# Optimization experiments

Hardware: AMD Instinct MI355X
Metric: run time of the kernel (lower is better)

## Reference

```python
import jax, jax.numpy as jnp
import numpy as np

N = 100000   # nodes
E = 1600000  # edges (avg degree 16)
IN = 128
HID = 128


def _init_params(key):
    ks = jax.random.split(key, 3)
    def glorot(k, fan_in, fan_out):
        s = (6.0 / (fan_in + fan_out)) ** 0.5
        return jax.random.uniform(k, (fan_in, fan_out), jnp.float32, -s, s)
    W1 = glorot(ks[0], IN, HID)
    W_mu = glorot(ks[1], HID, HID)
    W_lv = glorot(ks[2], HID, HID)
    b1 = jnp.zeros((HID,), jnp.float32)
    b_mu = jnp.zeros((HID,), jnp.float32)
    b_lv = jnp.zeros((HID,), jnp.float32)
    return W1, b1, W_mu, b_mu, W_lv, b_lv


def setup_inputs() -> dict:
    key = jax.random.key(0)
    k_x, k_e, k_p = jax.random.split(key, 3)
    x = jax.random.normal(k_x, (N, IN), jnp.float32)
    edge_index = jax.random.randint(k_e, (2, E), 0, N, jnp.int32)
    W1, b1, W_mu, b_mu, W_lv, b_lv = _init_params(k_p)
    return {"x": x, "edge_index": edge_index,
            "W1": W1, "b1": b1, "W_mu": W_mu, "b_mu": b_mu,
            "W_lv": W_lv, "b_lv": b_lv}


def _gcn_conv(x, src, dst, coef, self_coef, W, b):
    # PyG GCNConv: h = X W;  out_i = sum_j norm_ji * h_j  (incl. self loop) + b
    h = x @ W                                   # [N, H] dense GEMM
    msg = h[src] * coef[:, None]                # gather + scale  [E, H]
    agg = jnp.zeros_like(h).at[dst].add(msg)    # scatter-add      [N, H]
    agg = agg + h * self_coef[:, None]          # self-loop contribution
    return agg + b


def reference(x, edge_index, W1, b1, W_mu, b_mu, W_lv, b_lv):
    src, dst = edge_index[0], edge_index[1]
    n = x.shape[0]
    # symmetric norm with self loops: deg_i = in_degree_i + 1
    deg = jnp.zeros((n,), x.dtype).at[dst].add(1.0) + 1.0
    dinv = jax.lax.rsqrt(deg)
    coef = dinv[src] * dinv[dst]                # per-edge norm
    self_coef = dinv * dinv                     # per-node self-loop norm

    h = jax.nn.elu(_gcn_conv(x, src, dst, coef, self_coef, W1, b1))
    mu = _gcn_conv(h, src, dst, coef, self_coef, W_mu, b_mu)
    logvar = _gcn_conv(h, src, dst, coef, self_coef, W_lv, b_lv)

    # reparameterize: z = mu + eps * exp(0.5*logvar)
    eps = jax.random.normal(jax.random.key(42), mu.shape, mu.dtype)
    z = mu + eps * jnp.exp(0.5 * logvar)
    return z, mu, logvar
```

## Files before the change

kernel.cpp:

```cpp
#include <hip/hip_runtime.h>
#include <hip/hip_bf16.h>
#include <cstring>
#include <cstdint>

#define N_NODES 100000
#define N_EDGES 1600000
#define HID 128
#define TOT (N_NODES * HID)
#define GEMM_GRID_C 782
#define SCAT_GRID_C 6250



__device__ __forceinline__ float2 ld2(const float* p) { return *(const float2*)p; }
__device__ __forceinline__ float2 ld2(const __hip_bfloat16* p) {
    const __hip_bfloat162 h = *(const __hip_bfloat162*)p;
    return make_float2(__bfloat162float(h.x), __bfloat162float(h.y));
}

__device__ __forceinline__ void store8(float* p, const float* v) {
    *(float4*)(p)     = make_float4(v[0], v[1], v[2], v[3]);
    *(float4*)(p + 4) = make_float4(v[4], v[5], v[6], v[7]);
}
__device__ __forceinline__ void store8(__hip_bfloat16* p, const float* v) {
    union { unsigned short us[8]; uint4 q; } u;
#pragma unroll
    for (int i = 0; i < 8; ++i) {
        __hip_bfloat16 b = __float2bfloat16(v[i]);
        unsigned short raw;
        memcpy(&raw, &b, 2);
        u.us[i] = raw;
    }
    *(uint4*)p = u.q;
}

__global__ void k_count_rank(const int* __restrict__ dst, int* __restrict__ counts,
                             int* __restrict__ rank) {
    int e = blockIdx.x * 256 + threadIdx.x;
    if (e < N_EDGES) rank[e] = atomicAdd(&counts[dst[e]], 1);
}

__global__ void k_scan_block(const int* __restrict__ counts, int* __restrict__ partial,
                             int* __restrict__ bsum) {
    __shared__ int s[256];
    int i = blockIdx.x * 256 + threadIdx.x;
    int v = (i < N_NODES) ? counts[i] : 0;
    s[threadIdx.x] = v;
    __syncthreads();
    for (int off = 1; off < 256; off <<= 1) {
        int t = (threadIdx.x >= off) ? s[threadIdx.x - off] : 0;
        __syncthreads();
        s[threadIdx.x] += t;
        __syncthreads();
    }
    if (i < N_NODES) partial[i] = s[threadIdx.x] - v;
    if (threadIdx.x == 255) bsum[blockIdx.x] = s[255];
}

__global__ void k_scan_sums(int* __restrict__ bsum, int nb) {
    __shared__ int s[512];
    int v = (threadIdx.x < nb) ? bsum[threadIdx.x] : 0;
    s[threadIdx.x] = v;
    __syncthreads();
    for (int off = 1; off < 512; off <<= 1) {
        int t = (threadIdx.x >= off) ? s[threadIdx.x - off] : 0;
        __syncthreads();
        s[threadIdx.x] += t;
        __syncthreads();
    }
    if (threadIdx.x < nb) bsum[threadIdx.x] = s[threadIdx.x] - v;
}

__global__ void k_finalize(const int* __restrict__ counts, const int* __restrict__ partial,
                           const int* __restrict__ bsum, int* __restrict__ offsets,
                           float* __restrict__ dinv) {
    int i = blockIdx.x * 256 + threadIdx.x;
    if (i < N_NODES) {
        int o = partial[i] + bsum[blockIdx.x];
        offsets[i] = o;
        dinv[i] = rsqrtf((float)(counts[i] + 1));
    }
    if (i == 0) offsets[N_NODES] = N_EDGES;
}

__global__ __launch_bounds__(256) void k_gemm1_scatter(
    const float* __restrict__ A, const float* __restrict__ W,
    __hip_bfloat16* __restrict__ out,
    const int* __restrict__ src, const int* __restrict__ dst,
    const int* __restrict__ rank, const int* __restrict__ offsets,
    const float* __restrict__ dinv, int2* __restrict__ sorted) {
    __shared__ float Wl[16][128];
    __shared__ float Al[128][16];

    if (blockIdx.x >= GEMM_GRID_C) {
        int e = (blockIdx.x - GEMM_GRID_C) * 256 + threadIdx.x;
        if (e < N_EDGES) {
            int s = src[e], d = dst[e];
            int pos = offsets[d] + rank[e];
            float c = dinv[s] * dinv[d];
            sorted[pos] = make_int2(s, __float_as_int(c));
        }
        return;
    }

    int t = threadIdx.x;
    int R = blockIdx.x * 128;
    int tx = t & 15, ty = t >> 4;
    int c0 = tx * 8;
    int r0 = ty * 8;
    float acc[8][8] = {};

    for (int k0 = 0; k0 < 128; k0 += 16) {
        {
            const float4* Wg = (const float4*)(W + k0 * 128);
            ((float4*)&Wl[0][0])[t] = Wg[t];
            ((float4*)&Wl[0][0])[t + 256] = Wg[t + 256];
        }
        {
#pragma unroll
            for (int ii = 0; ii < 2; ++ii) {
                int id = t + ii * 256;
                int row = id >> 2, c4 = (id & 3) * 4;
                int gr = R + row;
                float4 v = make_float4(0.f, 0.f, 0.f, 0.f);
                if (gr < N_NODES) v = *(const float4*)(A + (size_t)gr * HID + k0 + c4);
                *(float4*)(&Al[row][c4]) = v;
            }
        }
        __syncthreads();

#pragma unroll
        for (int kk4 = 0; kk4 < 4; ++kk4) {
            float4 av4[8];
#pragma unroll
            for (int j = 0; j < 8; ++j) av4[j] = *(const float4*)(&Al[r0 + j][kk4 * 4]);
            const float* av = (const float*)av4;
#pragma unroll
            for (int kk = 0; kk < 4; ++kk) {
                float4 b0 = *(const float4*)(&Wl[kk4 * 4 + kk][c0]);
                float4 b1 = *(const float4*)(&Wl[kk4 * 4 + kk][c0 + 4]);
#pragma unroll
                for (int j = 0; j < 8; ++j) {
                    float a = av[j * 4 + kk];
                    acc[j][0] = fmaf(a, b0.x, acc[j][0]);
                    acc[j][1] = fmaf(a, b0.y, acc[j][1]);
                    acc[j][2] = fmaf(a, b0.z, acc[j][2]);
                    acc[j][3] = fmaf(a, b0.w, acc[j][3]);
                    acc[j][4] = fmaf(a, b1.x, acc[j][4]);
                    acc[j][5] = fmaf(a, b1.y, acc[j][5]);
                    acc[j][6] = fmaf(a, b1.z, acc[j][6]);
                    acc[j][7] = fmaf(a, b1.w, acc[j][7]);
                }
            }
        }
        __syncthreads();
    }

#pragma unroll
    for (int j = 0; j < 8; ++j) {
        int gr = R + r0 + j;
        if (gr >= N_NODES) continue;
        float v[8];
#pragma unroll
        for (int c = 0; c < 8; ++c) v[c] = acc[j][c];
        store8(out + (size_t)gr * HID + c0, v);
    }
}


#define AGG_BATCH(U)                                                              \
    {                                                                             \
        int2 sv[U];                                                               \
        float2 xs[U];                                                             \
        _Pragma("unroll") for (int i = 0; i < U; ++i) sv[i] = sorted[e + i];      \
        _Pragma("unroll") for (int i = 0; i < U; ++i)                             \
            xs[i] = ld2(Xf + (size_t)sv[i].x * HID);                              \
        _Pragma("unroll") for (int i = 0; i < U; ++i) {                           \
            float c = __int_as_float(sv[i].y);                                    \
            a0 = fmaf(c, xs[i].x, a0);                                            \
            a1 = fmaf(c, xs[i].y, a1);                                            \
        }                                                                         \
        e += U;                                                                   \
    }

#define AGG_BATCH_CLAMPED(U)                                                      \
    {                                                                             \
        int2 sv[U];                                                               \
        float2 xs[U];                                                             \
        _Pragma("unroll") for (int i = 0; i < U; ++i) {                           \
            int ee = e + i;                                                       \
            sv[i] = sorted[(ee < e1) ? ee : (e1 - 1)];                            \
        }                                                                         \
        _Pragma("unroll") for (int i = 0; i < U; ++i)                             \
            xs[i] = ld2(Xf + (size_t)sv[i].x * HID);                              \
        _Pragma("unroll") for (int i = 0; i < U; ++i) {                           \
            float c = (e + i < e1) ? __int_as_float(sv[i].y) : 0.f;               \
            a0 = fmaf(c, xs[i].x, a0);                                            \
            a1 = fmaf(c, xs[i].y, a1);                                            \
        }                                                                         \
    }

#define AGG_CORE(XTYPE)                                                           \
    int node = (blockIdx.x * 256 + threadIdx.x) >> 6;                             \
    int lane = threadIdx.x & 63;                                                  \
    if (node >= N_NODES) return;                                                  \
    int f = lane * 2;                                                             \
    const XTYPE* __restrict__ Xf = X + f;                                         \
    float di = dinv[node];                                                        \
    float sc = di * di;                                                           \
    float2 xi = ld2(Xf + (size_t)node * HID);                                     \
    float a0 = sc * xi.x, a1 = sc * xi.y;                                         \
    int e = offsets[node], e1 = offsets[node + 1];                                \
    int rem = e1 - e;                                                             \
    while (rem >= 16) {                                                           \
        AGG_BATCH(16);                                                            \
        rem -= 16;                                                                \
    }                                                                             \
    if (rem > 8) {                                                                \
        AGG_BATCH_CLAMPED(16);                                                    \
    } else if (rem > 0) {                                                         \
        AGG_BATCH_CLAMPED(8);                                                     \
    }

__global__ __launch_bounds__(256) void k_agg_h(const __hip_bfloat16* __restrict__ X,
                                               const int* __restrict__ offsets,
                                               const int2* __restrict__ sorted,
                                               const float* __restrict__ dinv,
                                               const float* __restrict__ b1,
                                               __hip_bfloat16* __restrict__ out) {
    AGG_CORE(__hip_bfloat16)
    float v0 = a0 + b1[f];
    float v1 = a1 + b1[f + 1];
    v0 = (v0 > 0.f) ? v0 : expm1f(v0);
    v1 = (v1 > 0.f) ? v1 : expm1f(v1);
    __hip_bfloat162 hb;
    hb.x = __float2bfloat16(v0);
    hb.y = __float2bfloat16(v1);
    *(__hip_bfloat162*)(out + (size_t)node * HID + f) = hb;
}

__global__ __launch_bounds__(256) void k_agg_f32(const __hip_bfloat16* __restrict__ X,
                                                 const int* __restrict__ offsets,
                                                 const int2* __restrict__ sorted,
                                                 const float* __restrict__ dinv,
                                                 float* __restrict__ out) {
    AGG_CORE(__hip_bfloat16)
    *(float2*)(out + (size_t)node * HID + f) = make_float2(a0, a1);
}

__global__ __launch_bounds__(256) void k_gemm_pair(const float* __restrict__ A,
                                                   const float* __restrict__ Wmu,
                                                   const float* __restrict__ bmu,
                                                   const float* __restrict__ Wlv,
                                                   const float* __restrict__ blv,
                                                   float* __restrict__ mu,
                                                   float* __restrict__ lv) {
    __shared__ float Wl[16][128];
    __shared__ float Al[128][16];
    int which = (blockIdx.x >= GEMM_GRID_C);
    const float* __restrict__ W = which ? Wlv : Wmu;
    const float* __restrict__ bias = which ? blv : bmu;
    float* __restrict__ out = which ? lv : mu;
    int bx = which ? (blockIdx.x - GEMM_GRID_C) : blockIdx.x;

    int t = threadIdx.x;
    int R = bx * 128;
    int tx = t & 15, ty = t >> 4;
    int c0 = tx * 8;
    int r0 = ty * 8;
    float acc[8][8] = {};

    for (int k0 = 0; k0 < 128; k0 += 16) {
        {
            const float4* Wg = (const float4*)(W + k0 * 128);
            ((float4*)&Wl[0][0])[t] = Wg[t];
            ((float4*)&Wl[0][0])[t + 256] = Wg[t + 256];
        }
        {
#pragma unroll
            for (int ii = 0; ii < 2; ++ii) {
                int id = t + ii * 256;
                int row = id >> 2, c4 = (id & 3) * 4;
                int gr = R + row;
                float4 v = make_float4(0.f, 0.f, 0.f, 0.f);
                if (gr < N_NODES) v = *(const float4*)(A + (size_t)gr * HID + k0 + c4);
                *(float4*)(&Al[row][c4]) = v;
            }
        }
        __syncthreads();

#pragma unroll
        for (int kk4 = 0; kk4 < 4; ++kk4) {
            float4 av4[8];
#pragma unroll
            for (int j = 0; j < 8; ++j) av4[j] = *(const float4*)(&Al[r0 + j][kk4 * 4]);
            const float* av = (const float*)av4;
#pragma unroll
            for (int kk = 0; kk < 4; ++kk) {
                float4 b0 = *(const float4*)(&Wl[kk4 * 4 + kk][c0]);
                float4 b1 = *(const float4*)(&Wl[kk4 * 4 + kk][c0 + 4]);
#pragma unroll
                for (int j = 0; j < 8; ++j) {
                    float a = av[j * 4 + kk];
                    acc[j][0] = fmaf(a, b0.x, acc[j][0]);
                    acc[j][1] = fmaf(a, b0.y, acc[j][1]);
                    acc[j][2] = fmaf(a, b0.z, acc[j][2]);
                    acc[j][3] = fmaf(a, b0.w, acc[j][3]);
                    acc[j][4] = fmaf(a, b1.x, acc[j][4]);
                    acc[j][5] = fmaf(a, b1.y, acc[j][5]);
                    acc[j][6] = fmaf(a, b1.z, acc[j][6]);
                    acc[j][7] = fmaf(a, b1.w, acc[j][7]);
                }
            }
        }
        __syncthreads();
    }

    float bcol[8];
#pragma unroll
    for (int c = 0; c < 8; ++c) bcol[c] = bias[c0 + c];
#pragma unroll
    for (int j = 0; j < 8; ++j) {
        int gr = R + r0 + j;
        if (gr >= N_NODES) continue;
        float v[8];
#pragma unroll
        for (int c = 0; c < 8; ++c) v[c] = acc[j][c] + bcol[c];
        store8(out + (size_t)gr * HID + c0, v);
    }
}

__device__ __forceinline__ unsigned rotl32(unsigned x, int r) {
    return (x << r) | (x >> (32 - r));
}

__device__ __forceinline__ void threefry2x32(unsigned x0, unsigned x1, unsigned& o0,
                                             unsigned& o1) {
    const unsigned ks0 = 0u, ks1 = 42u, ks2 = 0x1BD11BDAu ^ 42u;
    x0 += ks0;
    x1 += ks1;
    x0 += x1; x1 = rotl32(x1, 13); x1 ^= x0;
    x0 += x1; x1 = rotl32(x1, 15); x1 ^= x0;
    x0 += x1; x1 = rotl32(x1, 26); x1 ^= x0;
    x0 += x1; x1 = rotl32(x1, 6);  x1 ^= x0;
    x0 += ks1; x1 += ks2 + 1u;
    x0 += x1; x1 = rotl32(x1, 17); x1 ^= x0;
    x0 += x1; x1 = rotl32(x1, 29); x1 ^= x0;
    x0 += x1; x1 = rotl32(x1, 16); x1 ^= x0;
    x0 += x1; x1 = rotl32(x1, 24); x1 ^= x0;
    x0 += ks2; x1 += ks0 + 2u;
    x0 += x1; x1 = rotl32(x1, 13); x1 ^= x0;
    x0 += x1; x1 = rotl32(x1, 15); x1 ^= x0;
    x0 += x1; x1 = rotl32(x1, 26); x1 ^= x0;
    x0 += x1; x1 = rotl32(x1, 6);  x1 ^= x0;
    x0 += ks0; x1 += ks1 + 3u;
    x0 += x1; x1 = rotl32(x1, 17); x1 ^= x0;
    x0 += x1; x1 = rotl32(x1, 29); x1 ^= x0;
    x0 += x1; x1 = rotl32(x1, 16); x1 ^= x0;
    x0 += x1; x1 = rotl32(x1, 24); x1 ^= x0;
    x0 += ks1; x1 += ks2 + 4u;
    x0 += x1; x1 = rotl32(x1, 13); x1 ^= x0;
    x0 += x1; x1 = rotl32(x1, 15); x1 ^= x0;
    x0 += x1; x1 = rotl32(x1, 26); x1 ^= x0;
    x0 += x1; x1 = rotl32(x1, 6);  x1 ^= x0;
    x0 += ks2; x1 += ks0 + 5u;
    o0 = x0;
    o1 = x1;
}

__device__ __forceinline__ float erfinv_f32(float x) {
    float w = -log1pf(-x * x);
    float p;
    if (w < 5.0f) {
        w -= 2.5f;
        p = 2.81022636e-08f;
        p = fmaf(p, w, 3.43273939e-07f);
        p = fmaf(p, w, -3.5233877e-06f);
        p = fmaf(p, w, -4.39150654e-06f);
        p = fmaf(p, w, 0.00021858087f);
        p = fmaf(p, w, -0.00125372503f);
        p = fmaf(p, w, -0.00417768164f);
        p = fmaf(p, w, 0.246640727f);
        p = fmaf(p, w, 1.50140941f);
    } else {
        w = sqrtf(w) - 3.0f;
        p = -0.000200214257f;
        p = fmaf(p, w, 0.000100950558f);
        p = fmaf(p, w, 0.00134934322f);
        p = fmaf(p, w, -0.00367342844f);
        p = fmaf(p, w, 0.00573950773f);
        p = fmaf(p, w, -0.0076224613f);
        p = fmaf(p, w, 0.00943887047f);
        p = fmaf(p, w, 1.00167406f);
        p = fmaf(p, w, 2.83297682f);
    }
    return p * x;
}

__global__ __launch_bounds__(256) void k_sample(const float* __restrict__ mu,
                                                const float* __restrict__ lv,
                                                float* __restrict__ z) {
    int j = blockIdx.x * 256 + threadIdx.x;
    if (j >= TOT) return;
    unsigned o0, o1;
    threefry2x32(0u, (unsigned)j, o0, o1);
    unsigned bits = o0 ^ o1;
    float f = __uint_as_float((bits >> 9) | 0x3f800000u) - 1.0f;
    float u = f * 2.0f - 0.99999994f;
    u = fmaxf(u, -0.99999994f);
    float eps = 1.41421356f * erfinv_f32(u);
    z[j] = fmaf(eps, expf(0.5f * lv[j]), mu[j]);
}

extern "C" void kernel_launch(void* const* d_in, const int* in_sizes, int n_in,
                              void* d_out, int out_size, void* d_ws, size_t ws_size,
                              hipStream_t stream) {
    const float* x = (const float*)d_in[0];
    const int* ei = (const int*)d_in[1];
    const float* W1 = (const float*)d_in[2];
    const float* b1 = (const float*)d_in[3];
    const float* Wmu = (const float*)d_in[4];
    const float* bmu = (const float*)d_in[5];
    const float* Wlv = (const float*)d_in[6];
    const float* blv = (const float*)d_in[7];

    float* z = (float*)d_out;
    float* mu = z + (size_t)TOT;
    float* lv = z + 2 * (size_t)TOT;

    char* ws = (char*)d_ws;
    float* aggbuf = (float*)(ws + 0ull);
    __hip_bfloat16* t1buf = (__hip_bfloat16*)(ws + 0ull);
    int* rank = (int*)(ws + 25600000ull);
    __hip_bfloat16* hbf = (__hip_bfloat16*)(ws + 51200000ull);
    int* counts = (int*)(ws + 76800000ull);
    int* partial = (int*)(ws + 77200000ull);
    int* bsum = (int*)(ws + 77600000ull);
    int* offsets = (int*)(ws + 77602048ull);
    float* dinv = (float*)(ws + 78402176ull);
    int2* sorted = (int2*)(ws + 78802176ull);

    const int* src = ei;
    const int* dst = ei + N_EDGES;

    const int NBLK = (N_NODES + 255) / 256;
    const int AGG_GRID = (N_NODES * 64 + 255) / 256;

    hipMemsetAsync(counts, 0, N_NODES * sizeof(int), stream);
    k_count_rank<<<SCAT_GRID_C, 256, 0, stream>>>(dst, counts, rank);
    k_scan_block<<<NBLK, 256, 0, stream>>>(counts, partial, bsum);
    k_scan_sums<<<1, 512, 0, stream>>>(bsum, NBLK);
    k_finalize<<<NBLK, 256, 0, stream>>>(counts, partial, bsum, offsets, dinv);

    k_gemm1_scatter<<<GEMM_GRID_C + SCAT_GRID_C, 256, 0, stream>>>(
        x, W1, t1buf, src, dst, rank, offsets, dinv, sorted);

    k_agg_h<<<AGG_GRID, 256, 0, stream>>>(t1buf, offsets, sorted, dinv, b1, hbf);

    k_agg_f32<<<AGG_GRID, 256, 0, stream>>>(hbf, offsets, sorted, dinv, aggbuf);
    k_gemm_pair<<<2 * GEMM_GRID_C, 256, 0, stream>>>(aggbuf, Wmu, bmu, Wlv, blv, mu, lv);

    k_sample<<<(TOT + 255) / 256, 256, 0, stream>>>(mu, lv, z);
}
```

Before: 621.5 us.

## Use bf16 MFMA for mu/logvar GEMMs with bf16 aggregated input

The second-layer aggregation now writes bf16 instead of fp32, which halves that intermediate buffer's write and read traffic. The paired mu/logvar GEMM is replaced by a kernel built on 16x16x32 bf16 MFMA instructions. It loads A fragments and pre-transposed bf16 weights directly from global memory, with no LDS. A small prep kernel converts and transposes Wmu and Wlv to bf16 on every call. The cost is reduced precision on both the aggregated activations and the weights, plus uncoalesced scalar fp32 output stores.

Result: faster. 585.6 us (-5.8%).

```diff
diff --git a/kernel.cpp b/kernel.cpp
--- a/kernel.cpp
+++ b/kernel.cpp
@@ -11,6 +11,9 @@
 #define SCAT_GRID_C 6250
 
 
+
+typedef __bf16 bf16x8 __attribute__((ext_vector_type(8)));
+typedef float f32x4 __attribute__((ext_vector_type(4)));
 
 __device__ __forceinline__ float2 ld2(const float* p) { return *(const float2*)p; }
 __device__ __forceinline__ float2 ld2(const __hip_bfloat16* p) {
@@ -81,6 +84,17 @@
         dinv[i] = rsqrtf((float)(counts[i] + 1));
     }
     if (i == 0) offsets[N_NODES] = N_EDGES;
+}
+
+__global__ void k_prep_w(const float* __restrict__ Wmu, const float* __restrict__ Wlv,
+                         __hip_bfloat16* __restrict__ wmu_t,
+                         __hip_bfloat16* __restrict__ wlv_t) {
+    int idx = blockIdx.x * 256 + threadIdx.x;
+    if (idx < 128 * 128) {
+        int k = idx >> 7, n = idx & 127;
+        wmu_t[n * 128 + k] = __float2bfloat16(Wmu[idx]);
+        wlv_t[n * 128 + k] = __float2bfloat16(Wlv[idx]);
+    }
 }
 
 __global__ __launch_bounds__(256) void k_gemm1_scatter(
@@ -166,7 +180,6 @@
         store8(out + (size_t)gr * HID + c0, v);
     }
 }
-
 
 #define AGG_BATCH(U)                                                              \
     {                                                                             \
@@ -239,94 +252,80 @@
     *(__hip_bfloat162*)(out + (size_t)node * HID + f) = hb;
 }
 
-__global__ __launch_bounds__(256) void k_agg_f32(const __hip_bfloat16* __restrict__ X,
-                                                 const int* __restrict__ offsets,
-                                                 const int2* __restrict__ sorted,
-                                                 const float* __restrict__ dinv,
-                                                 float* __restrict__ out) {
+__global__ __launch_bounds__(256) void k_agg_bf16(const __hip_bfloat16* __restrict__ X,
+                                                  const int* __restrict__ offsets,
+                                                  const int2* __restrict__ sorted,
+                                                  const float* __restrict__ dinv,
+                                                  __hip_bfloat16* __restrict__ out) {
     AGG_CORE(__hip_bfloat16)
-    *(float2*)(out + (size_t)node * HID + f) = make_float2(a0, a1);
-}
-
-__global__ __launch_bounds__(256) void k_gemm_pair(const float* __restrict__ A,
-                                                   const float* __restrict__ Wmu,
-                                                   const float* __restrict__ bmu,
-                                                   const float* __restrict__ Wlv,
-                                                   const float* __restrict__ blv,
-                                                   float* __restrict__ mu,
-                                                   float* __restrict__ lv) {
-    __shared__ float Wl[16][128];
-    __shared__ float Al[128][16];
+    __hip_bfloat162 hb;
+    hb.x = __float2bfloat16(a0);
+    hb.y = __float2bfloat16(a1);
+    *(__hip_bfloat162*)(out + (size_t)node * HID + f) = hb;
+}
+
+__global__ __launch_bounds__(256) void k_gemm_pair_mfma(
+    const __hip_bfloat16* __restrict__ A,
+    const __hip_bfloat16* __restrict__ wmu_t, const float* __restrict__ bmu,
+    const __hip_bfloat16* __restrict__ wlv_t, const float* __restrict__ blv,
+    float* __restrict__ mu, float* __restrict__ lv) {
     int which = (blockIdx.x >= GEMM_GRID_C);
-    const float* __restrict__ W = which ? Wlv : Wmu;
+    const __hip_bfloat16* __restrict__ wt = which ? wlv_t : wmu_t;
     const float* __restrict__ bias = which ? blv : bmu;
     float* __restrict__ out = which ? lv : mu;
     int bx = which ? (blockIdx.x - GEMM_GRID_C) : blockIdx.x;
 
-    int t = threadIdx.x;
-    int R = bx * 128;
-    int tx = t & 15, ty = t >> 4;
-    int c0 = tx * 8;
-    int r0 = ty * 8;
-    float acc[8][8] = {};
-
-    for (int k0 = 0; k0 < 128; k0 += 16) {
-        {
-            const float4* Wg = (const float4*)(W + k0 * 128);
-            ((float4*)&Wl[0][0])[t] = Wg[t];
-            ((float4*)&Wl[0][0])[t + 256] = Wg[t + 256];
-        }
-        {
-#pragma unroll
-            for (int ii = 0; ii < 2; ++ii) {
-                int id = t + ii * 256;
-                int row = id >> 2, c4 = (id & 3) * 4;
-                int gr = R + row;
-                float4 v = make_float4(0.f, 0.f, 0.f, 0.f);
-                if (gr < N_NODES) v = *(const float4*)(A + (size_t)gr * HID + k0 + c4);
-                *(float4*)(&Al[row][c4]) = v;
+    int w = threadIdx.x >> 6;
+    int l = threadIdx.x & 63;
+    int l16 = l & 15, lg = l >> 4;
+    int wrow = bx * 128 + w * 32;
+
+    bf16x8 a[2][4];
+#pragma unroll
+    for (int mt = 0; mt < 2; ++mt) {
+#pragma unroll
+        for (int ks = 0; ks < 4; ++ks) {
+            int row = wrow + mt * 16 + l16;
+            int rr = (row < N_NODES) ? row : (N_NODES - 1);
+            a[mt][ks] = *reinterpret_cast<const bf16x8*>(
+                A + (size_t)rr * HID + ks * 32 + lg * 8);
+        }
+    }
+
+    f32x4 acc[2][8];
+#pragma unroll
+    for (int mt = 0; mt < 2; ++mt)
+#pragma unroll
+        for (int nt = 0; nt < 8; ++nt) acc[mt][nt] = (f32x4){0.f, 0.f, 0.f, 0.f};
+
+#pragma unroll
+    for (int nt = 0; nt < 8; ++nt) {
+        bf16x8 b[4];
+#pragma unroll
+        for (int ks = 0; ks < 4; ++ks)
+            b[ks] = *reinterpret_cast<const bf16x8*>(
+                wt + (size_t)(nt * 16 + l16) * HID + ks * 32 + lg * 8);
+#pragma unroll
+        for (int ks = 0; ks < 4; ++ks) {
+            acc[0][nt] = __builtin_amdgcn_mfma_f32_16x16x32_bf16(a[0][ks], b[ks],
+                                                                acc[0][nt], 0, 0, 0);
+            acc[1][nt] = __builtin_amdgcn_mfma_f32_16x16x32_bf16(a[1][ks], b[ks],
+                                                                acc[1][nt], 0, 0, 0);
+        }
+    }
+
+#pragma unroll
+    for (int nt = 0; nt < 8; ++nt) {
+        float bc = bias[nt * 16 + l16];
+#pragma unroll
+        for (int mt = 0; mt < 2; ++mt) {
+#pragma unroll
+            for (int r = 0; r < 4; ++r) {
+                int gr = wrow + mt * 16 + lg * 4 + r;
+                if (gr < N_NODES)
+                    out[(size_t)gr * HID + nt * 16 + l16] = acc[mt][nt][r] + bc;
             }
         }
-        __syncthreads();
-
-#pragma unroll
-        for (int kk4 = 0; kk4 < 4; ++kk4) {
-            float4 av4[8];
-#pragma unroll
-            for (int j = 0; j < 8; ++j) av4[j] = *(const float4*)(&Al[r0 + j][kk4 * 4]);
-            const float* av = (const float*)av4;
-#pragma unroll
-            for (int kk = 0; kk < 4; ++kk) {
-                float4 b0 = *(const float4*)(&Wl[kk4 * 4 + kk][c0]);
-                float4 b1 = *(const float4*)(&Wl[kk4 * 4 + kk][c0 + 4]);
-#pragma unroll
-                for (int j = 0; j < 8; ++j) {
-                    float a = av[j * 4 + kk];
-                    acc[j][0] = fmaf(a, b0.x, acc[j][0]);
-                    acc[j][1] = fmaf(a, b0.y, acc[j][1]);
-                    acc[j][2] = fmaf(a, b0.z, acc[j][2]);
-                    acc[j][3] = fmaf(a, b0.w, acc[j][3]);
-                    acc[j][4] = fmaf(a, b1.x, acc[j][4]);
-                    acc[j][5] = fmaf(a, b1.y, acc[j][5]);
-                    acc[j][6] = fmaf(a, b1.z, acc[j][6]);
-                    acc[j][7] = fmaf(a, b1.w, acc[j][7]);
-                }
-            }
-        }
-        __syncthreads();
-    }
-
-    float bcol[8];
-#pragma unroll
-    for (int c = 0; c < 8; ++c) bcol[c] = bias[c0 + c];
-#pragma unroll
-    for (int j = 0; j < 8; ++j) {
-        int gr = R + r0 + j;
-        if (gr >= N_NODES) continue;
-        float v[8];
-#pragma unroll
-        for (int c = 0; c < 8; ++c) v[c] = acc[j][c] + bcol[c];
-        store8(out + (size_t)gr * HID + c0, v);
     }
 }
 
@@ -429,14 +428,16 @@
     float* lv = z + 2 * (size_t)TOT;
 
     char* ws = (char*)d_ws;
-    float* aggbuf = (float*)(ws + 0ull);
     __hip_bfloat16* t1buf = (__hip_bfloat16*)(ws + 0ull);
+    __hip_bfloat16* habf = (__hip_bfloat16*)(ws + 0ull);
     int* rank = (int*)(ws + 25600000ull);
     __hip_bfloat16* hbf = (__hip_bfloat16*)(ws + 51200000ull);
     int* counts = (int*)(ws + 76800000ull);
     int* partial = (int*)(ws + 77200000ull);
     int* bsum = (int*)(ws + 77600000ull);
     int* offsets = (int*)(ws + 77602048ull);
+    __hip_bfloat16* wmu_t = (__hip_bfloat16*)(ws + 78002176ull);
+    __hip_bfloat16* wlv_t = (__hip_bfloat16*)(ws + 78034944ull);
     float* dinv = (float*)(ws + 78402176ull);
     int2* sorted = (int2*)(ws + 78802176ull);
 
@@ -447,6 +448,7 @@
     const int AGG_GRID = (N_NODES * 64 + 255) / 256;
 
     hipMemsetAsync(counts, 0, N_NODES * sizeof(int), stream);
+    k_prep_w<<<64, 256, 0, stream>>>(Wmu, Wlv, wmu_t, wlv_t);
     k_count_rank<<<SCAT_GRID_C, 256, 0, stream>>>(dst, counts, rank);
     k_scan_block<<<NBLK, 256, 0, stream>>>(counts, partial, bsum);
     k_scan_sums<<<1, 512, 0, stream>>>(bsum, NBLK);
@@ -457,8 +459,9 @@
 
     k_agg_h<<<AGG_GRID, 256, 0, stream>>>(t1buf, offsets, sorted, dinv, b1, hbf);
 
-    k_agg_f32<<<AGG_GRID, 256, 0, stream>>>(hbf, offsets, sorted, dinv, aggbuf);
-    k_gemm_pair<<<2 * GEMM_GRID_C, 256, 0, stream>>>(aggbuf, Wmu, bmu, Wlv, blv, mu, lv);
+    k_agg_bf16<<<AGG_GRID, 256, 0, stream>>>(hbf, offsets, sorted, dinv, habf);
+    k_gemm_pair_mfma<<<2 * GEMM_GRID_C, 256, 0, stream>>>(habf, wmu_t, bmu, wlv_t, blv,
+                                                          mu, lv);
 
     k_sample<<<(TOT + 255) / 256, 256, 0, stream>>>(mu, lv, z);
 }
```
